# Kernel tuning notes

Measured on AMD Instinct MI355X. Metric: run time of the kernel, lower is better.

The kernel has to match this reference:

```python
import jax, jax.numpy as jnp
import numpy as np

V, D, H, L, T_CTX = 50257, 768, 12, 12, 1024
HD = D // H
GELU_C = float(np.sqrt(2.0 / np.pi))


def new_gelu(x):
    return 0.5 * x * (1.0 + jnp.tanh(GELU_C * (x + 0.044715 * x ** 3)))


def layernorm(x, w, b, eps=1e-5):
    mu = jnp.mean(x, axis=-1, keepdims=True)
    var = jnp.var(x, axis=-1, keepdims=True)
    return (x - mu) * jax.lax.rsqrt(var + eps) * w + b


def setup_inputs() -> dict:
    key = jax.random.key(0)
    ks = jax.random.split(key, 20)
    B, T = 2, 1024
    s = 0.02
    inp = {
        "idx": jax.random.randint(ks[0], (B, T), 0, V),
        "targets": jax.random.randint(ks[1], (B, T), 0, V),
        "wte": jax.random.normal(ks[2], (V, D), jnp.float32) * s,
        "wpe": jax.random.normal(ks[3], (T_CTX, D), jnp.float32) * s,
        "ln1_w": jnp.ones((L, D)), "ln1_b": jnp.zeros((L, D)),
        "qkv_w": jax.random.normal(ks[4], (L, D, 3 * D), jnp.float32) * s,
        "qkv_b": jnp.zeros((L, 3 * D)),
        "proj_w": jax.random.normal(ks[5], (L, D, D), jnp.float32) * s,
        "proj_b": jnp.zeros((L, D)),
        "ln2_w": jnp.ones((L, D)), "ln2_b": jnp.zeros((L, D)),
        "fc_w": jax.random.normal(ks[6], (L, D, 4 * D), jnp.float32) * s,
        "fc_b": jnp.zeros((L, 4 * D)),
        "fc2_w": jax.random.normal(ks[7], (L, 4 * D, D), jnp.float32) * s,
        "fc2_b": jnp.zeros((L, D)),
        "lnf_w": jnp.ones((D,)), "lnf_b": jnp.zeros((D,)),
    }
    return inp


def _gpt_forward(idx, targets, wte, wpe, ln1_w, ln1_b, qkv_w, qkv_b, proj_w,
                 proj_b, ln2_w, ln2_b, fc_w, fc_b, fc2_w, fc2_b, lnf_w, lnf_b):
    B, T = idx.shape
    x = wte[idx] + wpe[:T]  # [B,T,D]
    scale = 1.0 / np.sqrt(HD)
    causal = jnp.tril(jnp.ones((T, T), dtype=bool))

    def block(x, p):
        l1w, l1b, qw, qb, pw, pb, l2w, l2b, fw, fb, f2w, f2b = p
        h = layernorm(x, l1w, l1b)
        qkv = h @ qw + qb  # [B,T,3D]
        q, k, v = jnp.split(qkv, 3, axis=-1)
        q = q.reshape(B, T, H, HD).transpose(0, 2, 1, 3)
        k = k.reshape(B, T, H, HD).transpose(0, 2, 1, 3)
        v = v.reshape(B, T, H, HD).transpose(0, 2, 1, 3)
        attn = jnp.einsum('bhqd,bhkd->bhqk', q, k) * scale
        attn = jnp.where(causal, attn, -jnp.inf)
        attn = jax.nn.softmax(attn, axis=-1)
        o = jnp.einsum('bhqk,bhkd->bhqd', attn, v)
        o = o.transpose(0, 2, 1, 3).reshape(B, T, D)
        x = x + (o @ pw + pb)
        h = layernorm(x, l2w, l2b)
        h = new_gelu(h @ fw + fb) @ f2w + f2b
        return x + h, None

    params = (ln1_w, ln1_b, qkv_w, qkv_b, proj_w, proj_b,
              ln2_w, ln2_b, fc_w, fc_b, fc2_w, fc2_b)
    x, _ = jax.lax.scan(block, x, params)
    x = layernorm(x, lnf_w, lnf_b)
    logits = x @ wte.T  # tied lm_head, [B,T,V]

    logp = jax.nn.log_softmax(logits, axis=-1)
    tflat = targets.reshape(-1)
    valid = tflat != -1
    tsafe = jnp.where(valid, tflat, 0)
    nll = -jnp.take_along_axis(logp.reshape(-1, V), tsafe[:, None], axis=-1)[:, 0]
    loss = jnp.sum(jnp.where(valid, nll, 0.0)) / jnp.maximum(jnp.sum(valid), 1)
    return logits, loss


def reference(idx, targets, wte, wpe, ln1_w, ln1_b, qkv_w, qkv_b, proj_w,
              proj_b, ln2_w, ln2_b, fc_w, fc_b, fc2_w, fc2_b, lnf_w, lnf_b):
    return _gpt_forward(idx, targets, wte, wpe, ln1_w, ln1_b, qkv_w, qkv_b,
                        proj_w, proj_b, ln2_w, ln2_b, fc_w, fc_b, fc2_w, fc2_b,
                        lnf_w, lnf_b)
```

## Files before the change

### kernel.cpp

```cpp
#include <hip/hip_runtime.h>
#include <hip/hip_bf16.h>
#include <math.h>

#define TT 1024
#define BB 2
#define DD 768
#define HH 12
#define NHD 64
#define LL 12
#define VV 50257
#define MROWS (BB*TT)
#define VPAD 50304
#define NT 393

typedef __attribute__((ext_vector_type(4))) float f32x4;
typedef __attribute__((ext_vector_type(8))) __bf16 bf16x8;
typedef __attribute__((ext_vector_type(8))) unsigned short u16x8;
typedef __hip_bfloat16 bf16;

__device__ __forceinline__ void gload_lds16(const bf16* g, bf16* l) {
    __builtin_amdgcn_global_load_lds((const __attribute__((address_space(1))) void*)g,
                                     (__attribute__((address_space(3))) void*)l, 16, 0, 0);
}

__global__ void embed_kernel(const int* __restrict__ idx, const float* __restrict__ wte,
                             const float* __restrict__ wpe, float* __restrict__ x) {
    int m = blockIdx.x;
    int t = m % TT;
    int tok = idx[m];
    const float* wrow = wte + (size_t)tok * DD;
    const float* prow = wpe + (size_t)t * DD;
    float* xrow = x + (size_t)m * DD;
    for (int c = threadIdx.x; c < DD; c += blockDim.x)
        xrow[c] = wrow[c] + prow[c];
}

__global__ void ln_kernel(const float* __restrict__ x, const float* __restrict__ w,
                          const float* __restrict__ b, bf16* __restrict__ out) {
    __shared__ float red[256];
    int m = blockIdx.x;
    int tid = threadIdx.x;
    const float* xr = x + (size_t)m * DD;
    float v0 = xr[tid], v1 = xr[tid + 256], v2 = xr[tid + 512];
    red[tid] = v0 + v1 + v2;
    __syncthreads();
    for (int s = 128; s > 0; s >>= 1) { if (tid < s) red[tid] += red[tid + s]; __syncthreads(); }
    float mu = red[0] * (1.0f / DD);
    __syncthreads();
    float d0 = v0 - mu, d1 = v1 - mu, d2 = v2 - mu;
    red[tid] = d0 * d0 + d1 * d1 + d2 * d2;
    __syncthreads();
    for (int s = 128; s > 0; s >>= 1) { if (tid < s) red[tid] += red[tid + s]; __syncthreads(); }
    float rstd = rsqrtf(red[0] * (1.0f / DD) + 1e-5f);
    bf16* orow = out + (size_t)m * DD;
    orow[tid]       = __float2bfloat16(d0 * rstd * w[tid]       + b[tid]);
    orow[tid + 256] = __float2bfloat16(d1 * rstd * w[tid + 256] + b[tid + 256]);
    orow[tid + 512] = __float2bfloat16(d2 * rstd * w[tid + 512] + b[tid + 512]);
}

__global__ void redln_kernel(const float* __restrict__ part, const float* __restrict__ bias,
                             const float* __restrict__ w, const float* __restrict__ b,
                             float* __restrict__ x, bf16* __restrict__ hb) {
    __shared__ float red[256];
    const size_t MN = (size_t)MROWS * DD;
    int m = blockIdx.x;
    int tid = threadIdx.x;
    float v[3];
    #pragma unroll
    for (int j = 0; j < 3; ++j) {
        int c = tid + j * 256;
        size_t i = (size_t)m * DD + c;
        v[j] = x[i] + part[i] + part[MN + i] + bias[c];
        x[i] = v[j];
    }
    red[tid] = v[0] + v[1] + v[2];
    __syncthreads();
    for (int s = 128; s > 0; s >>= 1) { if (tid < s) red[tid] += red[tid + s]; __syncthreads(); }
    float mu = red[0] * (1.0f / DD);
    __syncthreads();
    float d0 = v[0] - mu, d1 = v[1] - mu, d2 = v[2] - mu;
    red[tid] = d0 * d0 + d1 * d1 + d2 * d2;
    __syncthreads();
    for (int s = 128; s > 0; s >>= 1) { if (tid < s) red[tid] += red[tid + s]; __syncthreads(); }
    float rstd = rsqrtf(red[0] * (1.0f / DD) + 1e-5f);
    bf16* orow = hb + (size_t)m * DD;
    orow[tid]       = __float2bfloat16(d0 * rstd * w[tid]       + b[tid]);
    orow[tid + 256] = __float2bfloat16(d1 * rstd * w[tid + 256] + b[tid + 256]);
    orow[tid + 512] = __float2bfloat16(d2 * rstd * w[tid + 512] + b[tid + 512]);
}

__global__ void cast_kernel(const float* __restrict__ src, bf16* __restrict__ dst, int n4) {
    int stride = gridDim.x * blockDim.x;
    for (int i = blockIdx.x * blockDim.x + threadIdx.x; i < n4; i += stride) {
        float4 v = *(const float4*)(src + (size_t)i * 4);
        bf16* d = dst + (size_t)i * 4;
        d[0] = __float2bfloat16(v.x); d[1] = __float2bfloat16(v.y);
        d[2] = __float2bfloat16(v.z); d[3] = __float2bfloat16(v.w);
    }
}

__global__ void padzero_kernel(bf16* __restrict__ p, int n) {
    int i = blockIdx.x * 256 + threadIdx.x;
    if (i < n) p[i] = __float2bfloat16(0.f);
}

__global__ void tcast_kernel(const float* __restrict__ W, bf16* __restrict__ Wt,
                             int K, int N, size_t wstride, size_t tstride) {
    W  += (size_t)blockIdx.z * wstride;
    Wt += (size_t)blockIdx.z * tstride;
    __shared__ float t[32][33];
    int n0 = blockIdx.x * 32, k0 = blockIdx.y * 32;
    int c = threadIdx.x & 31, g = threadIdx.x >> 5;
    #pragma unroll
    for (int i = 0; i < 4; ++i) {
        int k = g * 4 + i;
        t[k][c] = W[(size_t)(k0 + k) * N + n0 + c];
    }
    __syncthreads();
    #pragma unroll
    for (int i = 0; i < 4; ++i) {
        int n = g * 4 + i;
        Wt[(size_t)(n0 + n) * K + k0 + c] = __float2bfloat16(t[c][n]);
    }
}

template<int BM, int BN, bool BIAS, bool GELU_, bool RES, bool OUTBF16, bool SPLITK>
__global__ __launch_bounds__(256, 3) void mgemm(
        const bf16* __restrict__ A, const bf16* __restrict__ Bm,
        const float* __restrict__ bias, const float* __restrict__ res,
        float* __restrict__ Cf, bf16* __restrict__ Cb, int M, int N, int K) {
    constexpr int WM = BM / 32, WN = BN / 32;
    constexpr int RA = BM / 32, RB = BN / 32;
    constexpr int NL = RA + RB;
    __shared__ __align__(16) bf16 As[2][BM * 64];
    __shared__ __align__(16) bf16 Bs[2][BN * 64];
    const int tid = threadIdx.x, lane = tid & 63, wid = tid >> 6;
    const int nbx = gridDim.x;
    const int nwg = nbx * gridDim.y;
    const int bidl = blockIdx.x + nbx * blockIdx.y;
    const int cpx = nwg >> 3;
    const int sw = (bidl & 7) * cpx + (bidl >> 3);
    const int m0 = (sw % nbx) * BM, n0 = (sw / nbx) * BN;
    const int wr = (wid >> 1) * (BM / 2), wc = (wid & 1) * (BN / 2);
    const int fr = lane & 15, fq = lane >> 4;

    const int Keff  = SPLITK ? (K >> 1) : K;
    const int kbase = SPLITK ? blockIdx.z * Keff : 0;
    if (SPLITK) Cf += (size_t)blockIdx.z * M * N;

    const int srow = tid >> 3;
    const int sk   = ((tid & 7) ^ (srow & 7)) * 8;
    const bf16* gA = A  + (size_t)(m0 + srow) * K + kbase + sk;
    const bf16* gB = Bm + (size_t)(n0 + srow) * K + kbase + sk;

    const int nt = Keff / 64;
    f32x4 acc[WM][WN] = {};

    auto stage = [&](int t) {
        bf16* dA = &As[t & 1][0] + tid * 8;
        bf16* dB = &Bs[t & 1][0] + tid * 8;
        const bf16* pA = gA + t * 64;
        const bf16* pB = gB + t * 64;
        #pragma unroll
        for (int u = 0; u < RA; ++u) gload_lds16(pA + (size_t)(u * 32) * K, dA + u * 2048);
        #pragma unroll
        for (int u = 0; u < RB; ++u) gload_lds16(pB + (size_t)(u * 32) * K, dB + u * 2048);
    };

    stage(0);

    for (int t = 0; t < nt; ++t) {
        if (t + 1 < nt) {
            stage(t + 1);
            asm volatile("s_waitcnt vmcnt(%0)" :: "i"(NL) : "memory");
        } else {
            asm volatile("s_waitcnt vmcnt(0)" ::: "memory");
        }
        __builtin_amdgcn_s_barrier();
        __builtin_amdgcn_sched_barrier(0);
        const bf16* abase = &As[t & 1][0];
        const bf16* bbase = &Bs[t & 1][0];
        #pragma unroll
        for (int ks = 0; ks < 2; ++ks) {
            const int kp = ((ks * 4 + fq) ^ (fr & 7)) * 8;
            bf16x8 af[WM], bq[WN];
            #pragma unroll
            for (int m = 0; m < WM; ++m)
                af[m] = *(const bf16x8*)(abase + (wr + m * 16 + fr) * 64 + kp);
            #pragma unroll
            for (int n = 0; n < WN; ++n)
                bq[n] = *(const bf16x8*)(bbase + (wc + n * 16 + fr) * 64 + kp);
            #pragma unroll
            for (int m = 0; m < WM; ++m)
                #pragma unroll
                for (int n = 0; n < WN; ++n)
                    acc[m][n] = __builtin_amdgcn_mfma_f32_16x16x32_bf16(af[m], bq[n], acc[m][n], 0, 0, 0);
        }
        __builtin_amdgcn_sched_barrier(0);
        __builtin_amdgcn_s_barrier();
    }

    #pragma unroll
    for (int m = 0; m < WM; ++m) {
        const int row = m0 + wr + m * 16 + fq * 4;
        #pragma unroll
        for (int n = 0; n < WN; ++n) {
            const int col = n0 + wc + n * 16 + fr;
            float bv = BIAS ? bias[col] : 0.f;
            #pragma unroll
            for (int r = 0; r < 4; ++r) {
                float v = acc[m][n][r] + bv;
                if (GELU_) {
                    float u = v;
                    float z = 1.5957691216057308f * (u + 0.044715f * u * u * u);
                    v = u / (1.0f + __expf(-z));
                }
                if (RES) v += res[(size_t)(row + r) * N + col];
                if (OUTBF16) Cb[(size_t)(row + r) * N + col] = __float2bfloat16(v);
                else         Cf[(size_t)(row + r) * N + col] = v;
            }
        }
    }
}

__global__ __launch_bounds__(256, 3) void mgemmL(
        const bf16* __restrict__ A, const bf16* __restrict__ Bm,
        float* __restrict__ Cf, float2* __restrict__ P, int N, int K) {
    constexpr int NL = 4;
    __shared__ __align__(16) bf16 As[2][128 * 32];
    __shared__ __align__(16) bf16 Bs[2][128 * 32];
    __shared__ float2 lbuf[4][64];
    const int tid = threadIdx.x, lane = tid & 63, wid = tid >> 6;
    const int nbx = gridDim.x;
    const int nwg = nbx * gridDim.y;
    const int bidl = blockIdx.x + nbx * blockIdx.y;
    const int cpx = nwg >> 3;
    const int sw = (bidl & 7) * cpx + (bidl >> 3);
    const int m0 = (sw % nbx) * 128, n0 = (sw / nbx) * 128;
    const int wr = (wid >> 1) * 64, wc = (wid & 1) * 64;
    const int fr = lane & 15, fq = lane >> 4;

    const int ksrc = ((lane & 3) ^ ((lane >> 3) & 3)) * 8;
    const bf16* gA = A  + (size_t)(m0 + wid * 16 + (lane >> 2)) * K + ksrc;
    const bf16* gB = Bm + (size_t)(n0 + wid * 16 + (lane >> 2)) * K + ksrc;
    bf16* lA = &As[0][0] + wid * 512 + lane * 8;
    bf16* lB = &Bs[0][0] + wid * 512 + lane * 8;
    const int kph = (fq ^ ((fr >> 1) & 3)) * 8;

    f32x4 acc[4][4] = {};
    const int nt = K / 32;

    #pragma unroll
    for (int i = 0; i < 2; ++i) gload_lds16(gA + (size_t)(i * 64) * K, lA + i * 2048);
    #pragma unroll
    for (int i = 0; i < 2; ++i) gload_lds16(gB + (size_t)(i * 64) * K, lB + i * 2048);

    for (int t = 0; t < nt; ++t) {
        const int cur = t & 1;
        if (t + 1 < nt) {
            const bf16* pA = gA + (t + 1) * 32;
            const bf16* pB = gB + (t + 1) * 32;
            bf16* dA = lA + (cur ^ 1) * (128 * 32);
            bf16* dB = lB + (cur ^ 1) * (128 * 32);
            #pragma unroll
            for (int i = 0; i < 2; ++i) gload_lds16(pA + (size_t)(i * 64) * K, dA + i * 2048);
            #pragma unroll
            for (int i = 0; i < 2; ++i) gload_lds16(pB + (size_t)(i * 64) * K, dB + i * 2048);
            asm volatile("s_waitcnt vmcnt(%0)" :: "i"(NL) : "memory");
        } else {
            asm volatile("s_waitcnt vmcnt(0)" ::: "memory");
        }
        __builtin_amdgcn_s_barrier();
        __builtin_amdgcn_sched_barrier(0);
        const bf16* abase = &As[cur][0];
        const bf16* bbase = &Bs[cur][0];
        bf16x8 af[4], bq[4];
        #pragma unroll
        for (int m = 0; m < 4; ++m)
            af[m] = *(const bf16x8*)(abase + (wr + m * 16 + fr) * 32 + kph);
        #pragma unroll
        for (int n = 0; n < 4; ++n)
            bq[n] = *(const bf16x8*)(bbase + (wc + n * 16 + fr) * 32 + kph);
        #pragma unroll
        for (int m = 0; m < 4; ++m)
            #pragma unroll
            for (int n = 0; n < 4; ++n)
                acc[m][n] = __builtin_amdgcn_mfma_f32_16x16x32_bf16(af[m], bq[n], acc[m][n], 0, 0, 0);
        __builtin_amdgcn_sched_barrier(0);
        __builtin_amdgcn_s_barrier();
    }

    #pragma unroll
    for (int m = 0; m < 4; ++m) {
        const int row = m0 + wr + m * 16 + fq * 4;
        #pragma unroll
        for (int n = 0; n < 4; ++n) {
            const int col = n0 + wc + n * 16 + fr;
            if (col < N) {
                #pragma unroll
                for (int r = 0; r < 4; ++r)
                    Cf[(size_t)(row + r) * N + col] = acc[m][n][r];
            }
        }
    }
    #pragma unroll
    for (int m = 0; m < 4; ++m) {
        #pragma unroll
        for (int r = 0; r < 4; ++r) {
            float mx = -1e30f;
            #pragma unroll
            for (int n = 0; n < 4; ++n) {
                int col = n0 + wc + n * 16 + fr;
                mx = fmaxf(mx, (col < N) ? acc[m][n][r] : -1e30f);
            }
            #pragma unroll
            for (int msk = 1; msk <= 8; msk <<= 1) mx = fmaxf(mx, __shfl_xor(mx, msk));
            float sm = 0.f;
            #pragma unroll
            for (int n = 0; n < 4; ++n) {
                int col = n0 + wc + n * 16 + fr;
                if (col < N) sm += __expf(acc[m][n][r] - mx);
            }
            #pragma unroll
            for (int msk = 1; msk <= 8; msk <<= 1) sm += __shfl_xor(sm, msk);
            if (fr == 0) lbuf[wid][m * 16 + fq * 4 + r] = make_float2(mx, sm);
        }
    }
    __syncthreads();
    if (tid < 128) {
        int half = tid >> 6, rl = tid & 63;
        float2 a = lbuf[half * 2][rl];
        float2 b = lbuf[half * 2 + 1][rl];
        float mc = fmaxf(a.x, b.x);
        float sc = a.y * __expf(a.x - mc) + b.y * __expf(b.x - mc);
        P[(size_t)(m0 + half * 64 + rl) * NT + (n0 >> 7)] = make_float2(mc, sc);
    }
}

__global__ __launch_bounds__(256) void attn3_kernel(const bf16* __restrict__ qkv,
                                                    bf16* __restrict__ out) {
    __shared__ bf16 Vt[64 * 64];
    __shared__ bf16 Ps[4][16 * 64];
    const int bid = blockIdx.x;
    const int q0 = (15 - (bid & 15)) * 64;
    const int h  = (bid / (TT / 64)) % HH;
    const int b  = bid / ((TT / 64) * HH);
    const int tid = threadIdx.x, lane = tid & 63, wid = tid >> 6;
    const int fr = lane & 15, fq = lane >> 4;
    const size_t rs = 3 * DD;

    bf16x8 qf[2];
    {
        const bf16* qb = qkv + (size_t)(b * TT + q0 + wid * 16 + fr) * rs + h * NHD;
        qf[0] = *(const bf16x8*)(qb + fq * 8);
        qf[1] = *(const bf16x8*)(qb + 32 + fq * 8);
    }
    float mrun[4] = {-1e30f, -1e30f, -1e30f, -1e30f};
    float lrun[4] = {0.f, 0.f, 0.f, 0.f};
    f32x4 o[4] = {};
    const int vrow = (tid & 31) * 2, kq = tid >> 5;
    const int ntile = q0 / 64 + 1;

    for (int jt = 0; jt < ntile; ++jt) {
        __syncthreads();
        {
            const u16x8* vb = (const u16x8*)(qkv + (size_t)(b * TT + jt * 64 + vrow) * rs + 2 * DD + h * NHD + kq * 8);
            u16x8 v0 = vb[0];
            u16x8 v1 = *(const u16x8*)((const bf16*)vb + rs);
            #pragma unroll
            for (int j = 0; j < 8; ++j) {
                int d = kq * 8 + j;
                int e = (d * 64 + vrow) ^ ((d & 7) << 3);
                *(unsigned int*)&Vt[e] = (unsigned int)v0[j] | ((unsigned int)v1[j] << 16);
            }
        }
        f32x4 s[4] = {};
        const bf16* kb = qkv + (size_t)(b * TT + jt * 64 + fr) * rs + DD + h * NHD;
        __builtin_amdgcn_s_setprio(1);
        #pragma unroll
        for (int n = 0; n < 4; ++n) {
            bf16x8 k0 = *(const bf16x8*)(kb + (size_t)(n * 16) * rs + fq * 8);
            bf16x8 k1 = *(const bf16x8*)(kb + (size_t)(n * 16) * rs + 32 + fq * 8);
            s[n] = __builtin_amdgcn_mfma_f32_16x16x32_bf16(qf[0], k0, s[n], 0, 0, 0);
            s[n] = __builtin_amdgcn_mfma_f32_16x16x32_bf16(qf[1], k1, s[n], 0, 0, 0);
        }
        __builtin_amdgcn_s_setprio(0);
        float mt[4] = {-1e30f, -1e30f, -1e30f, -1e30f};
        #pragma unroll
        for (int n = 0; n < 4; ++n) {
            int colg = jt * 64 + n * 16 + fr;
            #pragma unroll
            for (int r = 0; r < 4; ++r) {
                int rowg = q0 + wid * 16 + fq * 4 + r;
                float v = s[n][r] * 0.125f;
                if (colg > rowg) v = -1e30f;
                s[n][r] = v;
                mt[r] = fmaxf(mt[r], v);
            }
        }
        #pragma unroll
        for (int msk = 1; msk <= 8; msk <<= 1)
            #pragma unroll
            for (int r = 0; r < 4; ++r) mt[r] = fmaxf(mt[r], __shfl_xor(mt[r], msk));
        float sc[4], pt[4] = {0.f, 0.f, 0.f, 0.f};
        #pragma unroll
        for (int r = 0; r < 4; ++r) {
            float mn = fmaxf(mrun[r], mt[r]);
            sc[r] = __expf(mrun[r] - mn);
            mrun[r] = mn;
        }
        #pragma unroll
        for (int n = 0; n < 4; ++n)
            #pragma unroll
            for (int r = 0; r < 4; ++r) {
                float p = __expf(s[n][r] - mrun[r]);
                s[n][r] = p;
                pt[r] += p;
            }
        #pragma unroll
        for (int msk = 1; msk <= 8; msk <<= 1)
            #pragma unroll
            for (int r = 0; r < 4; ++r) pt[r] += __shfl_xor(pt[r], msk);
        #pragma unroll
        for (int r = 0; r < 4; ++r) lrun[r] = lrun[r] * sc[r] + pt[r];
        #pragma unroll
        for (int n2 = 0; n2 < 4; ++n2)
            #pragma unroll
            for (int r = 0; r < 4; ++r) o[n2][r] *= sc[r];
        #pragma unroll
        for (int n = 0; n < 4; ++n)
            #pragma unroll
            for (int r = 0; r < 4; ++r) {
                int row = fq * 4 + r;
                int e = (row * 64 + n * 16 + fr) ^ ((row & 7) << 3);
                Ps[wid][e] = __float2bfloat16(s[n][r]);
            }
        __syncthreads();
        __builtin_amdgcn_s_setprio(1);
        #pragma unroll
        for (int ks = 0; ks < 2; ++ks) {
            int pe = (fr * 64 + ks * 32 + fq * 8) ^ ((fr & 7) << 3);
            bf16x8 pa = *(const bf16x8*)&Ps[wid][pe];
            #pragma unroll
            for (int n2 = 0; n2 < 4; ++n2) {
                int d = n2 * 16 + fr;
                int ve = (d * 64 + ks * 32 + fq * 8) ^ ((d & 7) << 3);
                bf16x8 vv = *(const bf16x8*)&Vt[ve];
                o[n2] = __builtin_amdgcn_mfma_f32_16x16x32_bf16(pa, vv, o[n2], 0, 0, 0);
            }
        }
        __builtin_amdgcn_s_setprio(0);
    }
    #pragma unroll
    for (int r = 0; r < 4; ++r) {
        float inv = 1.f / lrun[r];
        bf16* op = out + (size_t)(b * TT + q0 + wid * 16 + fq * 4 + r) * DD + h * NHD;
        #pragma unroll
        for (int n2 = 0; n2 < 4; ++n2)
            op[n2 * 16 + fr] = __float2bfloat16(o[n2][r] * inv);
    }
}

__global__ void zero_kernel(float* p) { if (threadIdx.x == 0) p[0] = 0.f; }

__global__ void loss_finish(const float2* __restrict__ P, const float* __restrict__ logits,
                            const int* __restrict__ targets, float* __restrict__ acc) {
    __shared__ float rm[256], rs[256];
    int m = blockIdx.x;
    int tid = threadIdx.x;
    float mx = -1e30f, sm = 0.f;
    for (int i = tid; i < NT; i += 256) {
        float2 p = P[(size_t)m * NT + i];
        float nm = fmaxf(mx, p.x);
        sm = sm * __expf(mx - nm) + p.y * __expf(p.x - nm);
        mx = nm;
    }
    rm[tid] = mx; rs[tid] = sm;
    __syncthreads();
    for (int s = 128; s > 0; s >>= 1) {
        if (tid < s) {
            float m2 = rm[tid + s], s2 = rs[tid + s];
            float nm = fmaxf(rm[tid], m2);
            rs[tid] = rs[tid] * __expf(rm[tid] - nm) + s2 * __expf(m2 - nm);
            rm[tid] = nm;
        }
        __syncthreads();
    }
    if (tid == 0) {
        float lse = logf(rs[0]) + rm[0];
        atomicAdd(acc, lse - logits[(size_t)m * VV + targets[m]]);
    }
}

__global__ void loss_final(const float* __restrict__ acc, float* __restrict__ out) {
    if (threadIdx.x == 0) out[0] = acc[0] * (1.0f / (float)MROWS);
}

extern "C" void kernel_launch(void* const* d_in, const int* in_sizes, int n_in,
                              void* d_out, int out_size, void* d_ws, size_t ws_size,
                              hipStream_t stream) {
    const int*   idx     = (const int*)d_in[0];
    const int*   targets = (const int*)d_in[1];
    const float* wte     = (const float*)d_in[2];
    const float* wpe     = (const float*)d_in[3];
    const float* ln1_w   = (const float*)d_in[4];
    const float* ln1_b   = (const float*)d_in[5];
    const float* qkv_w   = (const float*)d_in[6];
    const float* qkv_b   = (const float*)d_in[7];
    const float* proj_w  = (const float*)d_in[8];
    const float* proj_b  = (const float*)d_in[9];
    const float* ln2_w   = (const float*)d_in[10];
    const float* ln2_b   = (const float*)d_in[11];
    const float* fc_w    = (const float*)d_in[12];
    const float* fc_b    = (const float*)d_in[13];
    const float* fc2_w   = (const float*)d_in[14];
    const float* fc2_b   = (const float*)d_in[15];
    const float* lnf_w   = (const float*)d_in[16];
    const float* lnf_b   = (const float*)d_in[17];

    float* logits = (float*)d_out;
    float* loss_out = logits + (size_t)MROWS * VV;

    const size_t LQ = (size_t)3 * DD * DD, LP = (size_t)DD * DD;
    const size_t LF = (size_t)4 * DD * DD, LF2 = (size_t)4 * DD * DD;
    const size_t LSTRIDE = LQ + LP + LF + LF2;

    float* x    = (float*)d_ws;
    float* lacc = x + (size_t)MROWS * DD;
    float* part = lacc + 16;
    bf16* qkvbuf = (bf16*)(part + (size_t)2 * MROWS * DD);
    bf16* hb   = qkvbuf + (size_t)MROWS * 3 * DD;
    bf16* ab   = hb + (size_t)MROWS * DD;
    bf16* gb   = ab + (size_t)MROWS * DD;
    bf16* wteb = gb + (size_t)MROWS * 4 * DD;
    bf16* wbase = wteb + (size_t)VPAD * DD;

    const size_t fixed_bytes = (size_t)((char*)wbase - (char*)d_ws);
    const bool hoist = ws_size >= fixed_bytes + sizeof(bf16) * LSTRIDE * LL;

    dim3 blk(256);
    cast_kernel<<<2048, blk, 0, stream>>>(wte, wteb, VV * DD / 4);
    padzero_kernel<<<((VPAD - VV) * DD + 255) / 256, blk, 0, stream>>>(
        wteb + (size_t)VV * DD, (VPAD - VV) * DD);
    embed_kernel<<<MROWS, blk, 0, stream>>>(idx, wte, wpe, x);

    if (hoist) {
        tcast_kernel<<<dim3(3 * DD / 32, DD / 32, LL), blk, 0, stream>>>(
            qkv_w, wbase, DD, 3 * DD, LQ, LSTRIDE);
        tcast_kernel<<<dim3(DD / 32, DD / 32, LL), blk, 0, stream>>>(
            proj_w, wbase + LQ, DD, DD, LP, LSTRIDE);
        tcast_kernel<<<dim3(4 * DD / 32, DD / 32, LL), blk, 0, stream>>>(
            fc_w, wbase + LQ + LP, DD, 4 * DD, LF, LSTRIDE);
        tcast_kernel<<<dim3(DD / 32, 4 * DD / 32, LL), blk, 0, stream>>>(
            fc2_w, wbase + LQ + LP + LF, 4 * DD, DD, LF2, LSTRIDE);
    }

    ln_kernel<<<MROWS, blk, 0, stream>>>(x, ln1_w, ln1_b, hb);

    for (int l = 0; l < LL; ++l) {
        bf16* wl = hoist ? wbase + (size_t)l * LSTRIDE : wbase;
        bf16* wQT = wl, *wPT = wl + LQ, *wFT = wl + LQ + LP, *wF2T = wl + LQ + LP + LF;
        if (!hoist) {
            tcast_kernel<<<dim3(3 * DD / 32, DD / 32, 1), blk, 0, stream>>>(qkv_w + (size_t)l * LQ, wQT, DD, 3 * DD, 0, 0);
            tcast_kernel<<<dim3(DD / 32, DD / 32, 1), blk, 0, stream>>>(proj_w + (size_t)l * LP, wPT, DD, DD, 0, 0);
            tcast_kernel<<<dim3(4 * DD / 32, DD / 32, 1), blk, 0, stream>>>(fc_w + (size_t)l * LF, wFT, DD, 4 * DD, 0, 0);
            tcast_kernel<<<dim3(DD / 32, 4 * DD / 32, 1), blk, 0, stream>>>(fc2_w + (size_t)l * LF2, wF2T, 4 * DD, DD, 0, 0);
        }

        mgemm<128, 64, true, false, false, true, false><<<dim3(MROWS / 128, 3 * DD / 64), blk, 0, stream>>>(
            hb, wQT, qkv_b + (size_t)l * 3 * DD, nullptr, nullptr, qkvbuf, MROWS, 3 * DD, DD);

        attn3_kernel<<<BB * HH * (TT / 64), blk, 0, stream>>>(qkvbuf, ab);

        mgemm<64, 64, false, false, false, false, true><<<dim3(MROWS / 64, DD / 64, 2), blk, 0, stream>>>(
            ab, wPT, nullptr, nullptr, part, nullptr, MROWS, DD, DD);
        redln_kernel<<<MROWS, blk, 0, stream>>>(part, proj_b + (size_t)l * DD,
            ln2_w + (size_t)l * DD, ln2_b + (size_t)l * DD, x, hb);

        mgemm<128, 64, true, true, false, true, false><<<dim3(MROWS / 128, 4 * DD / 64), blk, 0, stream>>>(
            hb, wFT, fc_b + (size_t)l * 4 * DD, nullptr, nullptr, gb, MROWS, 4 * DD, DD);

        mgemm<64, 64, false, false, false, false, true><<<dim3(MROWS / 64, DD / 64, 2), blk, 0, stream>>>(
            gb, wF2T, nullptr, nullptr, part, nullptr, MROWS, DD, 4 * DD);
        const float* nw = (l + 1 < LL) ? ln1_w + (size_t)(l + 1) * DD : lnf_w;
        const float* nb = (l + 1 < LL) ? ln1_b + (size_t)(l + 1) * DD : lnf_b;
        redln_kernel<<<MROWS, blk, 0, stream>>>(part, fc2_b + (size_t)l * DD, nw, nb, x, hb);
    }

    mgemmL<<<dim3(MROWS / 128, VPAD / 128), blk, 0, stream>>>(
        hb, wteb, logits, (float2*)part, VV, DD);

    zero_kernel<<<1, 64, 0, stream>>>(lacc);
    loss_finish<<<MROWS, blk, 0, stream>>>((const float2*)part, logits, targets, lacc);
    loss_final<<<1, 64, 0, stream>>>(lacc, loss_out);
}
```

Measured before the change: 2.363 ms.

## Enlarge LM-head GEMM tile to 256x128 with 512-thread workgroups

```diff
diff --git a/kernel.cpp b/kernel.cpp
--- a/kernel.cpp
+++ b/kernel.cpp
@@ -223,57 +223,55 @@
     }
 }
 
-__global__ __launch_bounds__(256, 3) void mgemmL(
+__global__ __launch_bounds__(512, 4) void mgemmL(
         const bf16* __restrict__ A, const bf16* __restrict__ Bm,
         float* __restrict__ Cf, float2* __restrict__ P, int N, int K) {
-    constexpr int NL = 4;
-    __shared__ __align__(16) bf16 As[2][128 * 32];
+    constexpr int NL = 3;
+    __shared__ __align__(16) bf16 As[2][256 * 32];
     __shared__ __align__(16) bf16 Bs[2][128 * 32];
-    __shared__ float2 lbuf[4][64];
+    __shared__ float2 lbuf[8][64];
     const int tid = threadIdx.x, lane = tid & 63, wid = tid >> 6;
     const int nbx = gridDim.x;
     const int nwg = nbx * gridDim.y;
     const int bidl = blockIdx.x + nbx * blockIdx.y;
     const int cpx = nwg >> 3;
     const int sw = (bidl & 7) * cpx + (bidl >> 3);
-    const int m0 = (sw % nbx) * 128, n0 = (sw / nbx) * 128;
-    const int wr = (wid >> 1) * 64, wc = (wid & 1) * 64;
+    const int m0 = (sw % nbx) * 256, n0 = (sw / nbx) * 128;
+    const int wm = wid >> 1, wn = wid & 1;
+    const int wr = wm * 64, wc = wn * 64;
     const int fr = lane & 15, fq = lane >> 4;
 
-    const int ksrc = ((lane & 3) ^ ((lane >> 3) & 3)) * 8;
-    const bf16* gA = A  + (size_t)(m0 + wid * 16 + (lane >> 2)) * K + ksrc;
-    const bf16* gB = Bm + (size_t)(n0 + wid * 16 + (lane >> 2)) * K + ksrc;
-    bf16* lA = &As[0][0] + wid * 512 + lane * 8;
-    bf16* lB = &Bs[0][0] + wid * 512 + lane * 8;
+    const int srow = tid >> 2;
+    const int ksrc = ((tid & 3) ^ ((tid >> 3) & 3)) * 8;
+    const bf16* gA = A  + (size_t)(m0 + srow) * K + ksrc;
+    const bf16* gB = Bm + (size_t)(n0 + srow) * K + ksrc;
     const int kph = (fq ^ ((fr >> 1) & 3)) * 8;
 
     f32x4 acc[4][4] = {};
     const int nt = K / 32;
 
-    #pragma unroll
-    for (int i = 0; i < 2; ++i) gload_lds16(gA + (size_t)(i * 64) * K, lA + i * 2048);
-    #pragma unroll
-    for (int i = 0; i < 2; ++i) gload_lds16(gB + (size_t)(i * 64) * K, lB + i * 2048);
+    auto stage = [&](int t) {
+        bf16* dA = &As[t & 1][0] + tid * 8;
+        bf16* dB = &Bs[t & 1][0] + tid * 8;
+        const bf16* pA = gA + t * 32;
+        #pragma unroll
+        for (int u = 0; u < 2; ++u) gload_lds16(pA + (size_t)(u * 128) * K, dA + u * 4096);
+        gload_lds16(gB + t * 32, dB);
+    };
+
+    stage(0);
 
     for (int t = 0; t < nt; ++t) {
-        const int cur = t & 1;
         if (t + 1 < nt) {
-            const bf16* pA = gA + (t + 1) * 32;
-            const bf16* pB = gB + (t + 1) * 32;
-            bf16* dA = lA + (cur ^ 1) * (128 * 32);
-            bf16* dB = lB + (cur ^ 1) * (128 * 32);
-            #pragma unroll
-            for (int i = 0; i < 2; ++i) gload_lds16(pA + (size_t)(i * 64) * K, dA + i * 2048);
-            #pragma unroll
-            for (int i = 0; i < 2; ++i) gload_lds16(pB + (size_t)(i * 64) * K, dB + i * 2048);
+            stage(t + 1);
             asm volatile("s_waitcnt vmcnt(%0)" :: "i"(NL) : "memory");
         } else {
             asm volatile("s_waitcnt vmcnt(0)" ::: "memory");
         }
         __builtin_amdgcn_s_barrier();
         __builtin_amdgcn_sched_barrier(0);
-        const bf16* abase = &As[cur][0];
-        const bf16* bbase = &Bs[cur][0];
+        const bf16* abase = &As[t & 1][0];
+        const bf16* bbase = &Bs[t & 1][0];
         bf16x8 af[4], bq[4];
         #pragma unroll
         for (int m = 0; m < 4; ++m)
@@ -327,13 +325,13 @@
         }
     }
     __syncthreads();
-    if (tid < 128) {
-        int half = tid >> 6, rl = tid & 63;
-        float2 a = lbuf[half * 2][rl];
-        float2 b = lbuf[half * 2 + 1][rl];
+    if (tid < 256) {
+        int band = tid >> 6, rl = tid & 63;
+        float2 a = lbuf[band * 2][rl];
+        float2 b = lbuf[band * 2 + 1][rl];
         float mc = fmaxf(a.x, b.x);
         float sc = a.y * __expf(a.x - mc) + b.y * __expf(b.x - mc);
-        P[(size_t)(m0 + half * 64 + rl) * NT + (n0 >> 7)] = make_float2(mc, sc);
+        P[(size_t)(m0 + band * 64 + rl) * NT + (n0 >> 7)] = make_float2(mc, sc);
     }
 }
 
@@ -587,7 +585,7 @@
         redln_kernel<<<MROWS, blk, 0, stream>>>(part, fc2_b + (size_t)l * DD, nw, nb, x, hb);
     }
 
-    mgemmL<<<dim3(MROWS / 128, VPAD / 128), blk, 0, stream>>>(
+    mgemmL<<<dim3(MROWS / 256, VPAD / 128), dim3(512), 0, stream>>>(
         hb, wteb, logits, (float2*)part, VV, DD);
 
     zero_kernel<<<1, 64, 0, stream>>>(lacc);
```

After: 2.374 ms. About the same (+0.5%).
